# Kernel tuning notes

Hardware: AMD Instinct MI355X
Metric: run time of the kernel (lower is better)

The kernel has to match this reference:

```python
import jax, jax.numpy as jnp
import numpy as np

D_MODEL = 1024
N_HEADS = 16
HEAD_DIM = D_MODEL // N_HEADS
RSQRT = 1.0 / np.sqrt(HEAD_DIM).astype(np.float32)


def setup_inputs() -> dict:
    key = jax.random.key(0)
    k1, k2, k3 = jax.random.split(key, 3)
    bs, sl = 4, 2048
    x = jax.random.normal(k1, (bs, sl, D_MODEL), dtype=jnp.float32)
    # stored as (in, out) so forward is x @ w; same math as torch Linear (no bias)
    w_qkv = jax.random.normal(k2, (D_MODEL, 3 * D_MODEL), dtype=jnp.float32) * 0.02
    w_proj = jax.random.normal(k3, (D_MODEL, D_MODEL), dtype=jnp.float32) * 0.02
    return {"x": x, "w_qkv": w_qkv, "w_proj": w_proj}


def reference(x, w_qkv, w_proj):
    bs, sl, dm = x.shape
    qkv = x @ w_qkv                                   # (bs, sl, 3*dm)
    q, k, v = jnp.split(qkv, 3, axis=-1)
    # (bs, sl, n, hd) -> (bs, n, sl, hd)
    q = q.reshape(bs, sl, N_HEADS, HEAD_DIM).transpose(0, 2, 1, 3)
    k = k.reshape(bs, sl, N_HEADS, HEAD_DIM).transpose(0, 2, 1, 3)
    v = v.reshape(bs, sl, N_HEADS, HEAD_DIM).transpose(0, 2, 1, 3)
    attn = jnp.einsum("bnqd,bnkd->bnqk", q, k) * RSQRT  # (bs, n, sl, sl)
    causal = jnp.tril(jnp.ones((sl, sl), dtype=bool))
    attn = jnp.where(causal[None, None], attn, -jnp.inf)
    attn = jax.nn.softmax(attn, axis=-1)
    out = jnp.einsum("bnqk,bnkd->bnqd", attn, v)      # (bs, n, sl, hd)
    out = out.transpose(0, 2, 1, 3).reshape(bs, sl, dm)
    return out @ w_proj
```

## Files before the change

kernel.cpp:

```cpp
#include <hip/hip_runtime.h>
#include <stdint.h>
#include <math.h>

typedef __attribute__((ext_vector_type(8))) short short8;
typedef __attribute__((ext_vector_type(4))) float f32x4;
typedef __attribute__((ext_vector_type(16))) float f32x16;

#define DEV __device__ __forceinline__

DEV unsigned short f2bf(float f) {
  union { float f; unsigned int u; } v; v.f = f;
  return (unsigned short)((v.u + 0x7FFFu + ((v.u >> 16) & 1u)) >> 16);
}

DEV unsigned int pkbf(float a, float b) {
  unsigned int r;
  asm("v_cvt_pk_bf16_f32 %0, %1, %2" : "=v"(r) : "v"(a), "v"(b));
  return r;
}

#if __has_builtin(__builtin_amdgcn_permlane32_swap)
DEV float redsum32(float v) {
  typedef __attribute__((ext_vector_type(2))) unsigned int uint2v;
  union { float f; unsigned int u; } c; c.f = v;
  uint2v r = __builtin_amdgcn_permlane32_swap(c.u, c.u, false, false);
  union { unsigned int u; float f; } a, b; a.u = r[0]; b.u = r[1];
  return a.f + b.f;
}
#else
DEV float redsum32(float v) { return v + __shfl_xor(v, 32, 64); }
#endif

DEV void gld16(const void* g, void* lds) {
  __builtin_amdgcn_global_load_lds(
      (const __attribute__((address_space(1))) unsigned int*)g,
      (__attribute__((address_space(3))) unsigned int*)lds, 16, 0, 0);
}

__global__ __launch_bounds__(256) void cvt_bf16_kernel(
    const float* __restrict__ in, unsigned short* __restrict__ out, int n) {
  int i = (blockIdx.x * 256 + threadIdx.x) * 8;
  if (i >= n) return;
  const float4 a = *(const float4*)(in + i);
  const float4 b = *(const float4*)(in + i + 4);
  short8 o;
  o[0] = (short)f2bf(a.x); o[1] = (short)f2bf(a.y);
  o[2] = (short)f2bf(a.z); o[3] = (short)f2bf(a.w);
  o[4] = (short)f2bf(b.x); o[5] = (short)f2bf(b.y);
  o[6] = (short)f2bf(b.z); o[7] = (short)f2bf(b.w);
  *(short8*)(out + i) = o;
}

__global__ __launch_bounds__(256) void transpose_w_kernel(
    const float* __restrict__ in, unsigned short* __restrict__ out,
    int Kdim, int Ndim) {
  __shared__ float t[32][33];
  const int nb = blockIdx.x * 32, kb = blockIdx.y * 32;
  const int tx = threadIdx.x & 31, ty = threadIdx.x >> 5;
#pragma unroll
  for (int i = 0; i < 32; i += 8)
    t[ty + i][tx] = in[(size_t)(kb + ty + i) * Ndim + nb + tx];
  __syncthreads();
#pragma unroll
  for (int i = 0; i < 32; i += 8)
    out[(size_t)(nb + ty + i) * Kdim + kb + tx] = f2bf(t[tx][ty + i]);
}

__global__ __launch_bounds__(256) void transpose_v_kernel(
    const unsigned short* __restrict__ V, unsigned short* __restrict__ Vf) {
  __shared__ __align__(16) unsigned short t[64][72];
  const int bh = blockIdx.y, s0 = blockIdx.x * 64;
  const int tid = threadIdx.x;
  const unsigned short* src = V + ((size_t)bh * 2048 + s0) * 64;
#pragma unroll
  for (int pass = 0; pass < 2; ++pass) {
    int r = (tid >> 3) + pass * 32;
    short8 v = *(const short8*)(src + r * 64 + (tid & 7) * 8);
    *(short8*)(&t[r][(tid & 7) * 8]) = v;
  }
  __syncthreads();
  const int f = tid >> 6, lane = tid & 63;
  const int ql = lane & 31, h = lane >> 5, t2 = f >> 1, sl = f & 1;
  unsigned short* dstb = Vf + (size_t)bh * 131072 + (size_t)(s0 >> 5) * 2048;
#pragma unroll
  for (int ktl = 0; ktl < 2; ++ktl) {
    short8 v;
#pragma unroll
    for (int j = 0; j < 8; ++j) {
      const int u = h * 8 + j;
      const int gu = (u & 3) | ((u & 4) << 1) | ((u & 8) >> 1);
      v[j] = (short)t[ktl * 32 + sl * 16 + gu][t2 * 32 + ql];
    }
    *(short8*)(dstb + ktl * 2048 + f * 512 + lane * 8) = v;
  }
}

template<int M, int N, int K, int MODE>
__global__ __launch_bounds__(256)
void gemm_bt_kernel(const unsigned short* __restrict__ A,
                    const unsigned short* __restrict__ Bt,
                    unsigned short* __restrict__ Qd,
                    unsigned short* __restrict__ Kd,
                    unsigned short* __restrict__ Vd,
                    float* __restrict__ outC) {
  __shared__ __align__(16) unsigned short lsA[128 * 32];
  __shared__ __align__(16) unsigned short lsB[128 * 32];
  const int tid = threadIdx.x, wid = tid >> 6, lane = tid & 63;
  const int wr = wid >> 1, wc = wid & 1;
  constexpr int nx = N / 128;
  constexpr int nwg = (M / 128) * nx;
  static_assert(nwg % 8 == 0, "bijective XCD swizzle needs nwg % 8 == 0");
  int id = blockIdx.y * nx + blockIdx.x;
  id = (id & 7) * (nwg / 8) + (id >> 3);
  const int m0 = (id / nx) * 128, n0 = (id % nx) * 128;

  f32x4 acc[4][4] = {};

  const int rA = lane >> 2, kA = (lane & 3) * 8;
  for (int kt = 0; kt < K / 32; ++kt) {
    __syncthreads();
#pragma unroll
    for (int c = 0; c < 2; ++c) {
      const int q = c * 4 + wid;
      gld16(A  + (size_t)(m0 + q * 16 + rA) * K + kt * 32 + kA, lsA + q * 512);
      gld16(Bt + (size_t)(n0 + q * 16 + rA) * K + kt * 32 + kA, lsB + q * 512);
    }
    __syncthreads();
    short8 af[4], bfr[4];
#pragma unroll
    for (int i = 0; i < 4; ++i) {
      af[i]  = *(const short8*)(lsA + (wr * 64 + i * 16 + (lane & 15)) * 32 + (lane >> 4) * 8);
      bfr[i] = *(const short8*)(lsB + (wc * 64 + i * 16 + (lane & 15)) * 32 + (lane >> 4) * 8);
    }
#pragma unroll
    for (int i = 0; i < 4; ++i)
#pragma unroll
      for (int j = 0; j < 4; ++j)
        acc[i][j] = __builtin_amdgcn_mfma_f32_16x16x32_bf16(af[i], bfr[j], acc[i][j], 0, 0, 0);
  }

#pragma unroll
  for (int i = 0; i < 4; ++i) {
#pragma unroll
    for (int j = 0; j < 4; ++j) {
      const int rbase = m0 + wr * 64 + i * 16 + (lane >> 4) * 4;
      const int col = n0 + wc * 64 + j * 16 + (lane & 15);
      if constexpr (MODE == 0) {
        const int which = col >> 10, h = (col >> 6) & 15, d = col & 63;
        unsigned short* dst = which == 0 ? Qd : (which == 1 ? Kd : Vd);
        const float scale = which == 0 ? 0.18033688f : 1.0f;
        const int sd = d >> 4, hi = (d >> 3) & 1, jd = d & 7;
#pragma unroll
        for (int ii = 0; ii < 4; ++ii) {
          const int r = rbase + ii, b = r >> 11, seq = r & 2047;
          size_t idx;
          if (which == 2)
            idx = ((size_t)(b * 16 + h) * 2048 + seq) * 64 + d;
          else
            idx = ((((size_t)(b * 16 + h) * 64 + (seq >> 5)) * 4 + sd) * 64
                   + (seq & 31) + 32 * hi) * 8 + jd;
          dst[idx] = f2bf(acc[i][j][ii] * scale);
        }
      } else {
#pragma unroll
        for (int ii = 0; ii < 4; ++ii)
          outC[(size_t)(rbase + ii) * N + col] = acc[i][j][ii];
      }
    }
  }
}

DEV void loadK4f(const unsigned short* Kfb, int kt, int lane, short8 kf[4]) {
  const unsigned short* p = Kfb + (size_t)kt * 2048 + lane * 8;
#pragma unroll
  for (int s = 0; s < 4; ++s) kf[s] = *(const short8*)(p + s * 512);
}
DEV void loadV4f(const unsigned short* Vfb, int kt, int lane, short8 vf[4]) {
  const unsigned short* p = Vfb + (size_t)kt * 2048 + lane * 8;
#pragma unroll
  for (int f = 0; f < 4; ++f) vf[f] = *(const short8*)(p + f * 512);
}

template<int NP, bool MASK>
DEV void attn_step(int kv0, const short8 kf[4], const short8 qf[][4],
                   const int q0[], const short8 vf[4],
                   float l[], f32x16 o[][2], int ql, int h) {
  f32x16 st[NP];
  __builtin_amdgcn_s_setprio(1);
#pragma unroll
  for (int pp = 0; pp < NP; ++pp) {
    f32x16 s = {};
#pragma unroll
    for (int ss = 0; ss < 4; ++ss)
      s = __builtin_amdgcn_mfma_f32_32x32x16_bf16(kf[ss], qf[pp][ss], s, 0, 0, 0);
    st[pp] = s;
  }
  __builtin_amdgcn_s_setprio(0);
  if constexpr (MASK) {
#pragma unroll
    for (int r = 0; r < 16; ++r) {
      const int krow = (r & 3) + 8 * (r >> 2) + 4 * h;
      if (kv0 + krow > q0[0] + ql) st[0][r] = -INFINITY;
    }
  }
  union pk_t { unsigned int u[4]; short8 s8; };
  pk_t f0[NP], f1[NP];
#pragma unroll
  for (int pp = 0; pp < NP; ++pp) {
    float p[16];
#pragma unroll
    for (int r = 0; r < 16; ++r) p[r] = exp2f(fminf(st[pp][r], 64.f));
    float ps = ((p[0] + p[1]) + (p[2] + p[3])) + ((p[4] + p[5]) + (p[6] + p[7]));
    ps += ((p[8] + p[9]) + (p[10] + p[11])) + ((p[12] + p[13]) + (p[14] + p[15]));
    l[pp] += ps;
#pragma unroll
    for (int i = 0; i < 4; ++i) {
      f0[pp].u[i] = pkbf(p[2 * i], p[2 * i + 1]);
      f1[pp].u[i] = pkbf(p[8 + 2 * i], p[9 + 2 * i]);
    }
  }
  __builtin_amdgcn_s_setprio(1);
#pragma unroll
  for (int pp = 0; pp < NP; ++pp) {
    o[pp][0] = __builtin_amdgcn_mfma_f32_32x32x16_bf16(vf[0], f0[pp].s8, o[pp][0], 0, 0, 0);
    o[pp][0] = __builtin_amdgcn_mfma_f32_32x32x16_bf16(vf[1], f1[pp].s8, o[pp][0], 0, 0, 0);
    o[pp][1] = __builtin_amdgcn_mfma_f32_32x32x16_bf16(vf[2], f0[pp].s8, o[pp][1], 0, 0, 0);
    o[pp][1] = __builtin_amdgcn_mfma_f32_32x32x16_bf16(vf[3], f1[pp].s8, o[pp][1], 0, 0, 0);
  }
  __builtin_amdgcn_s_setprio(0);
}

__global__ __launch_bounds__(256, 2)
void attn_kernel(const unsigned short* __restrict__ Qf,
                 const unsigned short* __restrict__ Kf,
                 const unsigned short* __restrict__ Vf,
                 unsigned short* __restrict__ O) {
  const int bh = blockIdx.x & 63;
  const int w  = blockIdx.x >> 6;
  const int wid = threadIdx.x >> 6, lane = threadIdx.x & 63;
  const int ql = lane & 31, h = lane >> 5;
  const int qtA = w * 4 + wid;
  const int qtB = 63 - qtA;
  const int q0[2] = {qtA * 32, qtB * 32};

  const unsigned short* Qfb = Qf + (size_t)bh * 131072;
  const unsigned short* Kfb = Kf + (size_t)bh * 131072;
  const unsigned short* Vfb = Vf + (size_t)bh * 131072;

  short8 qf[2][4];
#pragma unroll
  for (int pp = 0; pp < 2; ++pp) {
    const int qt = pp == 0 ? qtA : qtB;
#pragma unroll
    for (int s = 0; s < 4; ++s)
      qf[pp][s] = *(const short8*)(Qfb + (size_t)qt * 2048 + s * 512 + lane * 8);
  }

  f32x16 o[2][2] = {};
  float l[2] = {0.f, 0.f};

  short8 kf[4], kn[4], vf[4];
  loadK4f(Kfb, 0, lane, kf);

  for (int t = 0; t < qtA; ++t) {
    loadV4f(Vfb, t, lane, vf);
    loadK4f(Kfb, t + 1, lane, kn);
    attn_step<2, false>(0, kf, qf, q0, vf, l, o, ql, h);
#pragma unroll
    for (int s = 0; s < 4; ++s) kf[s] = kn[s];
  }
  {
    loadV4f(Vfb, qtA, lane, vf);
    loadK4f(Kfb, qtA + 1, lane, kn);
    attn_step<2, true>(qtA * 32, kf, qf, q0, vf, l, o, ql, h);
#pragma unroll
    for (int s = 0; s < 4; ++s) kf[s] = kn[s];
  }
  for (int t = qtA + 1; t < qtB; ++t) {
    loadV4f(Vfb, t, lane, vf);
    loadK4f(Kfb, t + 1, lane, kn);
    attn_step<1, false>(0, kf, &qf[1], &q0[1], vf, &l[1], &o[1], ql, h);
#pragma unroll
    for (int s = 0; s < 4; ++s) kf[s] = kn[s];
  }
  {
    loadV4f(Vfb, qtB, lane, vf);
    attn_step<1, true>(qtB * 32, kf, &qf[1], &q0[1], vf, &l[1], &o[1], ql, h);
  }

  const int b = bh >> 4, head = bh & 15;
#pragma unroll
  for (int pp = 0; pp < 2; ++pp) {
    const float inv = 1.0f / redsum32(l[pp]);
    unsigned short* Orow = O + ((size_t)(b * 2048 + q0[pp] + ql)) * 1024 + head * 64;
#pragma unroll
    for (int g = 0; g < 4; ++g) {
      {
        const unsigned int lo = pkbf(o[pp][0][g * 4 + 0] * inv, o[pp][0][g * 4 + 1] * inv);
        const unsigned int hi = pkbf(o[pp][0][g * 4 + 2] * inv, o[pp][0][g * 4 + 3] * inv);
        uint2 val; val.x = lo; val.y = hi;
        *(uint2*)(Orow + 8 * g + 4 * h) = val;
      }
      {
        const unsigned int lo = pkbf(o[pp][1][g * 4 + 0] * inv, o[pp][1][g * 4 + 1] * inv);
        const unsigned int hi = pkbf(o[pp][1][g * 4 + 2] * inv, o[pp][1][g * 4 + 3] * inv);
        uint2 val; val.x = lo; val.y = hi;
        *(uint2*)(Orow + 32 + 8 * g + 4 * h) = val;
      }
    }
  }
}

extern "C" void kernel_launch(void* const* d_in, const int* in_sizes, int n_in,
                              void* d_out, int out_size, void* d_ws, size_t ws_size,
                              hipStream_t stream) {
  (void)in_sizes; (void)n_in; (void)out_size; (void)ws_size;
  const float* x      = (const float*)d_in[0];
  const float* w_qkv  = (const float*)d_in[1];
  const float* w_proj = (const float*)d_in[2];
  float* out = (float*)d_out;
  char* ws = (char*)d_ws;

  unsigned short* x_bf   = (unsigned short*)(ws);
  unsigned short* wqT    = (unsigned short*)(ws + 16777216);
  unsigned short* wpT    = (unsigned short*)(ws + 23068672);
  unsigned short* Qfd    = (unsigned short*)(ws + 25165824);
  unsigned short* Kfd    = (unsigned short*)(ws + 41943040);
  unsigned short* Vd     = (unsigned short*)(ws + 58720256);
  unsigned short* Vfd    = (unsigned short*)(ws + 75497472);
  unsigned short* attn_o = x_bf;

  cvt_bf16_kernel<<<4096, 256, 0, stream>>>(x, x_bf, 8388608);
  transpose_w_kernel<<<dim3(96, 32), 256, 0, stream>>>(w_qkv, wqT, 1024, 3072);
  transpose_w_kernel<<<dim3(32, 32), 256, 0, stream>>>(w_proj, wpT, 1024, 1024);
  gemm_bt_kernel<8192, 3072, 1024, 0><<<dim3(24, 64), 256, 0, stream>>>(
      x_bf, wqT, Qfd, Kfd, Vd, nullptr);
  transpose_v_kernel<<<dim3(32, 64), 256, 0, stream>>>(Vd, Vfd);
  attn_kernel<<<512, 256, 0, stream>>>(Qfd, Kfd, Vfd, attn_o);
  gemm_bt_kernel<8192, 1024, 1024, 1><<<dim3(8, 64), 256, 0, stream>>>(
      attn_o, wpT, nullptr, nullptr, nullptr, out);
}
```

Before: 185.6 us.

## Fuse V transpose into QKV GEMM epilogue and double K-step per barrier

Removes the separate transpose_v_kernel by having the QKV GEMM epilogue scatter V directly into the fragment layout the attention kernel expects. This saves one launch and a full read and write of V. The GEMM main loop also loads two 32-wide K slices per iteration into doubled LDS buffers, which halves the number of barrier pairs. LDS use doubles per block, and the scattered 2-byte stores in the V epilogue may coalesce poorly.

```diff
diff --git a/kernel.cpp b/kernel.cpp
--- a/kernel.cpp
+++ b/kernel.cpp
@@ -66,35 +66,6 @@
     out[(size_t)(nb + ty + i) * Kdim + kb + tx] = f2bf(t[tx][ty + i]);
 }
 
-__global__ __launch_bounds__(256) void transpose_v_kernel(
-    const unsigned short* __restrict__ V, unsigned short* __restrict__ Vf) {
-  __shared__ __align__(16) unsigned short t[64][72];
-  const int bh = blockIdx.y, s0 = blockIdx.x * 64;
-  const int tid = threadIdx.x;
-  const unsigned short* src = V + ((size_t)bh * 2048 + s0) * 64;
-#pragma unroll
-  for (int pass = 0; pass < 2; ++pass) {
-    int r = (tid >> 3) + pass * 32;
-    short8 v = *(const short8*)(src + r * 64 + (tid & 7) * 8);
-    *(short8*)(&t[r][(tid & 7) * 8]) = v;
-  }
-  __syncthreads();
-  const int f = tid >> 6, lane = tid & 63;
-  const int ql = lane & 31, h = lane >> 5, t2 = f >> 1, sl = f & 1;
-  unsigned short* dstb = Vf + (size_t)bh * 131072 + (size_t)(s0 >> 5) * 2048;
-#pragma unroll
-  for (int ktl = 0; ktl < 2; ++ktl) {
-    short8 v;
-#pragma unroll
-    for (int j = 0; j < 8; ++j) {
-      const int u = h * 8 + j;
-      const int gu = (u & 3) | ((u & 4) << 1) | ((u & 8) >> 1);
-      v[j] = (short)t[ktl * 32 + sl * 16 + gu][t2 * 32 + ql];
-    }
-    *(short8*)(dstb + ktl * 2048 + f * 512 + lane * 8) = v;
-  }
-}
-
 template<int M, int N, int K, int MODE>
 __global__ __launch_bounds__(256)
 void gemm_bt_kernel(const unsigned short* __restrict__ A,
@@ -103,8 +74,8 @@
                     unsigned short* __restrict__ Kd,
                     unsigned short* __restrict__ Vd,
                     float* __restrict__ outC) {
-  __shared__ __align__(16) unsigned short lsA[128 * 32];
-  __shared__ __align__(16) unsigned short lsB[128 * 32];
+  __shared__ __align__(16) unsigned short lsA[2][128 * 32];
+  __shared__ __align__(16) unsigned short lsB[2][128 * 32];
   const int tid = threadIdx.x, wid = tid >> 6, lane = tid & 63;
   const int wr = wid >> 1, wc = wid & 1;
   constexpr int nx = N / 128;
@@ -117,26 +88,33 @@
   f32x4 acc[4][4] = {};
 
   const int rA = lane >> 2, kA = (lane & 3) * 8;
-  for (int kt = 0; kt < K / 32; ++kt) {
+  for (int kt = 0; kt < K / 64; ++kt) {
     __syncthreads();
 #pragma unroll
     for (int c = 0; c < 2; ++c) {
       const int q = c * 4 + wid;
-      gld16(A  + (size_t)(m0 + q * 16 + rA) * K + kt * 32 + kA, lsA + q * 512);
-      gld16(Bt + (size_t)(n0 + q * 16 + rA) * K + kt * 32 + kA, lsB + q * 512);
+      const size_t ar = (size_t)(m0 + q * 16 + rA) * K + kt * 64 + kA;
+      const size_t br = (size_t)(n0 + q * 16 + rA) * K + kt * 64 + kA;
+      gld16(A  + ar,      lsA[0] + q * 512);
+      gld16(A  + ar + 32, lsA[1] + q * 512);
+      gld16(Bt + br,      lsB[0] + q * 512);
+      gld16(Bt + br + 32, lsB[1] + q * 512);
     }
     __syncthreads();
-    short8 af[4], bfr[4];
-#pragma unroll
-    for (int i = 0; i < 4; ++i) {
-      af[i]  = *(const short8*)(lsA + (wr * 64 + i * 16 + (lane & 15)) * 32 + (lane >> 4) * 8);
-      bfr[i] = *(const short8*)(lsB + (wc * 64 + i * 16 + (lane & 15)) * 32 + (lane >> 4) * 8);
-    }
-#pragma unroll
-    for (int i = 0; i < 4; ++i)
-#pragma unroll
-      for (int j = 0; j < 4; ++j)
-        acc[i][j] = __builtin_amdgcn_mfma_f32_16x16x32_bf16(af[i], bfr[j], acc[i][j], 0, 0, 0);
+#pragma unroll
+    for (int kk = 0; kk < 2; ++kk) {
+      short8 af[4], bfr[4];
+#pragma unroll
+      for (int i = 0; i < 4; ++i) {
+        af[i]  = *(const short8*)(lsA[kk] + (wr * 64 + i * 16 + (lane & 15)) * 32 + (lane >> 4) * 8);
+        bfr[i] = *(const short8*)(lsB[kk] + (wc * 64 + i * 16 + (lane & 15)) * 32 + (lane >> 4) * 8);
+      }
+#pragma unroll
+      for (int i = 0; i < 4; ++i)
+#pragma unroll
+        for (int j = 0; j < 4; ++j)
+          acc[i][j] = __builtin_amdgcn_mfma_f32_16x16x32_bf16(af[i], bfr[j], acc[i][j], 0, 0, 0);
+    }
   }
 
 #pragma unroll
@@ -146,19 +124,24 @@
       const int rbase = m0 + wr * 64 + i * 16 + (lane >> 4) * 4;
       const int col = n0 + wc * 64 + j * 16 + (lane & 15);
       if constexpr (MODE == 0) {
-        const int which = col >> 10, h = (col >> 6) & 15, d = col & 63;
+        const int which = col >> 10, hh = (col >> 6) & 15, d = col & 63;
         unsigned short* dst = which == 0 ? Qd : (which == 1 ? Kd : Vd);
         const float scale = which == 0 ? 0.18033688f : 1.0f;
         const int sd = d >> 4, hi = (d >> 3) & 1, jd = d & 7;
+        const int t2 = d >> 5, qlv = d & 31;
 #pragma unroll
         for (int ii = 0; ii < 4; ++ii) {
           const int r = rbase + ii, b = r >> 11, seq = r & 2047;
           size_t idx;
-          if (which == 2)
-            idx = ((size_t)(b * 16 + h) * 2048 + seq) * 64 + d;
-          else
-            idx = ((((size_t)(b * 16 + h) * 64 + (seq >> 5)) * 4 + sd) * 64
+          if (which == 2) {
+            const int kt2 = seq >> 5, sl = (seq >> 4) & 1, g = seq & 15;
+            const int u = (g & 3) | ((g & 4) << 1) | ((g & 8) >> 1);
+            idx = ((((size_t)(b * 16 + hh) * 64 + kt2) * 4 + (t2 * 2 + sl)) * 64
+                   + qlv + 32 * (u >> 3)) * 8 + (u & 7);
+          } else {
+            idx = ((((size_t)(b * 16 + hh) * 64 + (seq >> 5)) * 4 + sd) * 64
                    + (seq & 31) + 32 * hi) * 8 + jd;
+          }
           dst[idx] = f2bf(acc[i][j][ii] * scale);
         }
       } else {
@@ -326,16 +309,14 @@
   unsigned short* wpT    = (unsigned short*)(ws + 23068672);
   unsigned short* Qfd    = (unsigned short*)(ws + 25165824);
   unsigned short* Kfd    = (unsigned short*)(ws + 41943040);
-  unsigned short* Vd     = (unsigned short*)(ws + 58720256);
-  unsigned short* Vfd    = (unsigned short*)(ws + 75497472);
+  unsigned short* Vfd    = (unsigned short*)(ws + 58720256);
   unsigned short* attn_o = x_bf;
 
   cvt_bf16_kernel<<<4096, 256, 0, stream>>>(x, x_bf, 8388608);
   transpose_w_kernel<<<dim3(96, 32), 256, 0, stream>>>(w_qkv, wqT, 1024, 3072);
   transpose_w_kernel<<<dim3(32, 32), 256, 0, stream>>>(w_proj, wpT, 1024, 1024);
   gemm_bt_kernel<8192, 3072, 1024, 0><<<dim3(24, 64), 256, 0, stream>>>(
-      x_bf, wqT, Qfd, Kfd, Vd, nullptr);
-  transpose_v_kernel<<<dim3(32, 64), 256, 0, stream>>>(Vd, Vfd);
+      x_bf, wqT, Qfd, Kfd, Vfd, nullptr);
   attn_kernel<<<512, 256, 0, stream>>>(Qfd, Kfd, Vfd, attn_o);
   gemm_bt_kernel<8192, 1024, 1024, 1><<<dim3(8, 64), 256, 0, stream>>>(
       attn_o, wpT, nullptr, nullptr, nullptr, out);
```

Result: faster. 175.1 us (-5.7%).
